# Kernel optimization log

Measured on AMD Instinct MI355X. Metric: run time of the kernel, lower is better.

## Reference

```python
import jax, jax.numpy as jnp
import numpy as np

B, T, D, H, E, O = 4, 2048, 512, 2048, 4, 512
C = 1024  # expert capacity
HE = H // E  # per-expert hidden width


def setup_inputs() -> dict:
    key = jax.random.key(0)
    ks = jax.random.split(key, 7)
    x = jax.random.normal(ks[0], (B, T, D), dtype=jnp.float32)
    dispatch_mask = jax.random.uniform(ks[1], (B, T, E, C), dtype=jnp.float32)
    combine_array = jax.random.uniform(ks[2], (B, T, E, C), dtype=jnp.float32)
    # per-expert parameters (fc1 contract, fc2 expand)
    w1 = jax.random.normal(ks[3], (E, D, HE), dtype=jnp.float32) * (1.0 / np.sqrt(D))
    b1 = jnp.zeros((E, HE), dtype=jnp.float32)
    w2 = jax.random.normal(ks[4], (E, HE, O), dtype=jnp.float32) * (1.0 / np.sqrt(HE))
    b2 = jnp.zeros((O,), dtype=jnp.float32)
    return {"x": x, "dispatch_mask": dispatch_mask, "combine_array": combine_array,
            "w1": w1, "b1": b1, "w2": w2, "b2": b2}


def reference(x, dispatch_mask, combine_array, w1, b1, w2, b2):
    # dispatch: gather tokens into per-expert capacity buffers [B,E,C,D]
    xd = jnp.einsum('btd,btec->becd', x, dispatch_mask)
    # per-expert fc1: [B,E,C,HE]
    h = jnp.einsum('becd,edh->bech', xd, w1) + b1[None, :, None, :]
    # GELU (exact erf form, matching torch nn.GELU default); norm/dropout are identity
    h = jax.nn.gelu(h, approximate=False)
    # per-expert fc2: [B,E,C,O]
    y = jnp.einsum('bech,eho->beco', h, w2)
    # combine: scatter expert outputs back to tokens [B,T,O]
    out = jnp.einsum('beco,btec->bto', y, combine_array) + b2
    return out
```

## Files before the change

### kernel.cpp

```cpp
#include <hip/hip_runtime.h>
#include <math.h>

namespace {

typedef short short8 __attribute__((ext_vector_type(8)));
typedef float f32x4 __attribute__((ext_vector_type(4)));

constexpr int kB = 4, kT = 2048, kD = 512, kE = 4, kC = 1024, kHE = 512,
              kO = 512, kEC = 4096;

__device__ __forceinline__ unsigned short f2bf(float f) {
    unsigned int u = __float_as_uint(f);
    u += 0x7fffu + ((u >> 16) & 1u);
    return (unsigned short)(u >> 16);
}

__device__ __forceinline__ float gelu_exact(float v) {
    return 0.5f * v * (1.0f + erff(v * 0.70710678118654752f));
}

#define GLDS16(g, l)                                                      \
    __builtin_amdgcn_global_load_lds(                                     \
        (const __attribute__((address_space(1))) unsigned int*)(g),       \
        (__attribute__((address_space(3))) unsigned int*)(l), 16, 0, 0)

__global__ __launch_bounds__(256)
void transpose_cast(const float* __restrict__ in, unsigned short* __restrict__ out,
                    int R, int Cc, long long sIn, long long sOut)
{
    __shared__ float tile[32][33];
    const int z = blockIdx.z;
    const float* ip = in + (long long)z * sIn;
    unsigned short* op = out + (long long)z * sOut;
    const int c0 = blockIdx.x * 32, r0 = blockIdx.y * 32;
    const int tx = threadIdx.x & 31, ty = threadIdx.x >> 5;
#pragma unroll
    for (int i = 0; i < 4; ++i) {
        const int r = ty + i * 8;
        tile[r][tx] = ip[(size_t)(r0 + r) * Cc + c0 + tx];
    }
    __syncthreads();
#pragma unroll
    for (int i = 0; i < 4; ++i) {
        const int c = ty + i * 8;
        op[(size_t)(c0 + c) * R + r0 + tx] = f2bf(tile[tx][c]);
    }
}

__global__ __launch_bounds__(256)
void cast_bf16(const float* __restrict__ in, unsigned short* __restrict__ out,
               long long n)
{
    const long long i = ((long long)blockIdx.x * blockDim.x + threadIdx.x) * 4;
    if (i < n) {
        const float4 v = *(const float4*)&in[i];
        unsigned short o[4] = {f2bf(v.x), f2bf(v.y), f2bf(v.z), f2bf(v.w)};
        *(uint2*)&out[i] = *(const uint2*)o;
    }
}

template <int MODE>
__global__ __launch_bounds__(256)
void mfma_gemm(const unsigned short* __restrict__ Aall,
               const unsigned short* __restrict__ Ball,
               const float* __restrict__ biasAll,
               void* __restrict__ Call,
               int M, int N, int K,
               long long sA, long long sB, long long sC,
               int zModA, int zModB, int zModBias, int biasStride, int bShift)
{
    __shared__ unsigned short As[128 * 64];
    __shared__ unsigned short Bs[128 * 64];

    const int z = blockIdx.z;
    const unsigned short* Ab = Aall + (long long)(z % zModA) * sA;
    const unsigned short* Bb = Ball + (long long)(z % zModB) * sB;
    const float* bias =
        (MODE != 0) ? biasAll + (long long)(z % zModBias) * biasStride : nullptr;

    const int t = threadIdx.x;
    const int lane = t & 63;
    const int w = t >> 6;
    const int wrow = w * 32;
    const int l8r = lane >> 3;
    const int l8c = (lane & 7) * 8;
    const int row0 = blockIdx.y * 128;
    const int col0 = blockIdx.x * 128;

    const int wm = (w >> 1) * 64;
    const int wn = (w & 1) * 64;
    const int fr = lane & 15;
    const int fq = (lane >> 4) * 8;

    const unsigned int bMask = (1u << bShift) - 1u;

    f32x4 acc[4][4] = {};

    for (int k0 = 0; k0 < K; k0 += 64) {
#pragma unroll
        for (int r = 0; r < 4; ++r) {
            const int ar = row0 + wrow + r * 8 + l8r;
            GLDS16(Ab + (size_t)ar * K + (k0 + l8c), &As[(wrow + r * 8) * 64]);
            const int bn = col0 + wrow + r * 8 + l8r;
            const int gk = k0 + l8c;
            const size_t boff =
                (((size_t)(gk >> bShift) * N + bn) << bShift) + (gk & bMask);
            GLDS16(Bb + boff, &Bs[(wrow + r * 8) * 64]);
        }
        __syncthreads();
#pragma unroll
        for (int kk = 0; kk < 2; ++kk) {
            short8 af[4], bf[4];
#pragma unroll
            for (int i = 0; i < 4; ++i)
                af[i] = *(const short8*)&As[(wm + i * 16 + fr) * 64 + kk * 32 + fq];
#pragma unroll
            for (int j = 0; j < 4; ++j)
                bf[j] = *(const short8*)&Bs[(wn + j * 16 + fr) * 64 + kk * 32 + fq];
#pragma unroll
            for (int i = 0; i < 4; ++i)
#pragma unroll
                for (int j = 0; j < 4; ++j)
                    acc[i][j] = __builtin_amdgcn_mfma_f32_16x16x32_bf16(
                        af[i], bf[j], acc[i][j], 0, 0, 0);
        }
        __syncthreads();
    }

    const long long cz = (long long)z * sC;
#pragma unroll
    for (int i = 0; i < 4; ++i) {
        const int rowb = row0 + wm + i * 16 + (lane >> 4) * 4;
#pragma unroll
        for (int j = 0; j < 4; ++j) {
            const int col = col0 + wn + j * 16 + fr;
            const float bv = (MODE != 0) ? bias[col] : 0.0f;
#pragma unroll
            for (int r = 0; r < 4; ++r) {
                const float v = acc[i][j][r];
                const size_t idx = (size_t)cz + (size_t)(rowb + r) * N + col;
                if (MODE == 0)
                    ((unsigned short*)Call)[idx] = f2bf(v);
                else if (MODE == 1)
                    ((unsigned short*)Call)[idx] = f2bf(gelu_exact(v + bv));
                else
                    ((float*)Call)[idx] = v + bv;
            }
        }
    }
}

}

extern "C" void kernel_launch(void* const* d_in, const int* in_sizes, int n_in,
                              void* d_out, int out_size, void* d_ws, size_t ws_size,
                              hipStream_t stream)
{
    const float* x    = (const float*)d_in[0];
    const float* mask = (const float*)d_in[1];
    const float* comb = (const float*)d_in[2];
    const float* w1   = (const float*)d_in[3];
    const float* b1   = (const float*)d_in[4];
    const float* w2   = (const float*)d_in[5];
    const float* b2   = (const float*)d_in[6];
    float* out = (float*)d_out;

    unsigned short* ws    = (unsigned short*)d_ws;
    unsigned short* regA  = ws;
    unsigned short* xT    = regA + 33554432;
    unsigned short* w1T   = xT + 4194304;
    unsigned short* w2T   = w1T + 1048576;
    unsigned short* xd    = w2T + 1048576;
    unsigned short* h     = xd + 8388608;
    unsigned short* maskT = regA;
    unsigned short* combB = regA;
    unsigned short* yT    = xd;

    dim3 blk(256);

    transpose_cast<<<dim3(kEC / 32, kT / 32, kB), blk, 0, stream>>>(
        mask, maskT, kT, kEC, (long long)kT * kEC, (long long)kT * kEC);
    transpose_cast<<<dim3(kD / 32, kT / 32, kB), blk, 0, stream>>>(
        x, xT, kT, kD, (long long)kT * kD, (long long)kT * kD);
    transpose_cast<<<dim3(kHE / 32, kD / 32, kE), blk, 0, stream>>>(
        w1, w1T, kD, kHE, (long long)kD * kHE, (long long)kD * kHE);
    transpose_cast<<<dim3(kO / 32, kHE / 32, kE), blk, 0, stream>>>(
        w2, w2T, kHE, kO, (long long)kHE * kO, (long long)kHE * kO);

    mfma_gemm<0><<<dim3(kD / 128, kEC / 128, kB), blk, 0, stream>>>(
        maskT, xT, nullptr, xd, kEC, kD, kT,
        (long long)kEC * kT, (long long)kD * kT, (long long)kEC * kD,
        kB, kB, 1, 0, 11);

    cast_bf16<<<dim3(33554432 / 4 / 256), blk, 0, stream>>>(
        comb, combB, 33554432LL);

    mfma_gemm<1><<<dim3(kHE / 128, kC / 128, kB * kE), blk, 0, stream>>>(
        xd, w1T, b1, h, kC, kHE, kD,
        (long long)kC * kD, (long long)kHE * kD, (long long)kC * kHE,
        kB * kE, kE, kE, kHE, 9);

    mfma_gemm<0><<<dim3(kC / 128, kO / 128, kB * kE), blk, 0, stream>>>(
        w2T, h, nullptr, yT, kO, kC, kHE,
        (long long)kO * kHE, (long long)kC * kHE, (long long)kO * kC,
        kE, kB * kE, 1, 0, 9);

    mfma_gemm<3><<<dim3(kO / 128, kT / 128, kB), blk, 0, stream>>>(
        combB, yT, b2, out, kT, kO, kEC,
        (long long)kT * kEC, (long long)kE * kO * kC, (long long)kT * kO,
        kB, kB, 1, 0, 10);
}
```

Before: 500.3 us.

## Double-buffer GEMM LDS tiles with async prefetch and XOR-swizzled layout

Adds a second LDS buffer for the A and B tiles so the global-to-LDS loads for the next K tile are issued before computing the current one, with explicit vmcnt waits and raw barriers in place of __syncthreads. The LDS layout is also XOR-swizzled on the 16-byte column chunk to reduce bank conflicts on the MFMA fragment reads. Launch bounds request two blocks per CU. LDS use doubles to 64KB per block, which may limit occupancy, and the hand-written waitcnt counts must match the number of issued loads.

```diff
diff --git a/kernel.cpp b/kernel.cpp
--- a/kernel.cpp
+++ b/kernel.cpp
@@ -60,7 +60,7 @@
 }
 
 template <int MODE>
-__global__ __launch_bounds__(256)
+__global__ __launch_bounds__(256, 2)
 void mfma_gemm(const unsigned short* __restrict__ Aall,
                const unsigned short* __restrict__ Ball,
                const float* __restrict__ biasAll,
@@ -69,8 +69,8 @@
                long long sA, long long sB, long long sC,
                int zModA, int zModB, int zModBias, int biasStride, int bShift)
 {
-    __shared__ unsigned short As[128 * 64];
-    __shared__ unsigned short Bs[128 * 64];
+    __shared__ unsigned short As[2][128 * 64];
+    __shared__ unsigned short Bs[2][128 * 64];
 
     const int z = blockIdx.z;
     const unsigned short* Ab = Aall + (long long)(z % zModA) * sA;
@@ -83,7 +83,7 @@
     const int w = t >> 6;
     const int wrow = w * 32;
     const int l8r = lane >> 3;
-    const int l8c = (lane & 7) * 8;
+    const int l8c = ((lane & 7) ^ l8r) * 8;
     const int row0 = blockIdx.y * 128;
     const int col0 = blockIdx.x * 128;
 
@@ -91,32 +91,49 @@
     const int wn = (w & 1) * 64;
     const int fr = lane & 15;
     const int fq = (lane >> 4) * 8;
+    const int fsw = (fr & 7) * 8;
 
     const unsigned int bMask = (1u << bShift) - 1u;
 
     f32x4 acc[4][4] = {};
 
-    for (int k0 = 0; k0 < K; k0 += 64) {
-#pragma unroll
-        for (int r = 0; r < 4; ++r) {
-            const int ar = row0 + wrow + r * 8 + l8r;
-            GLDS16(Ab + (size_t)ar * K + (k0 + l8c), &As[(wrow + r * 8) * 64]);
-            const int bn = col0 + wrow + r * 8 + l8r;
-            const int gk = k0 + l8c;
-            const size_t boff =
-                (((size_t)(gk >> bShift) * N + bn) << bShift) + (gk & bMask);
-            GLDS16(Bb + boff, &Bs[(wrow + r * 8) * 64]);
+#define STAGE(buf, k0)                                                        \
+    do {                                                                      \
+        _Pragma("unroll")                                                     \
+        for (int r = 0; r < 4; ++r) {                                         \
+            const int ar = row0 + wrow + r * 8 + l8r;                         \
+            GLDS16(Ab + (size_t)ar * K + ((k0) + l8c),                        \
+                   &As[buf][(wrow + r * 8) * 64]);                            \
+            const int bn = col0 + wrow + r * 8 + l8r;                         \
+            const int gk = (k0) + l8c;                                        \
+            const size_t boff =                                               \
+                (((size_t)(gk >> bShift) * N + bn) << bShift) + (gk & bMask); \
+            GLDS16(Bb + boff, &Bs[buf][(wrow + r * 8) * 64]);                 \
+        }                                                                     \
+    } while (0)
+
+    const int nt = K / 64;
+    STAGE(0, 0);
+    int cur = 0;
+    for (int t0 = 0; t0 < nt; ++t0) {
+        if (t0 + 1 < nt) {
+            STAGE(cur ^ 1, (t0 + 1) * 64);
+            asm volatile("s_waitcnt vmcnt(8)" ::: "memory");
+        } else {
+            asm volatile("s_waitcnt vmcnt(0)" ::: "memory");
         }
-        __syncthreads();
+        __builtin_amdgcn_s_barrier();
 #pragma unroll
         for (int kk = 0; kk < 2; ++kk) {
             short8 af[4], bf[4];
 #pragma unroll
             for (int i = 0; i < 4; ++i)
-                af[i] = *(const short8*)&As[(wm + i * 16 + fr) * 64 + kk * 32 + fq];
+                af[i] = *(const short8*)&As[cur][(wm + i * 16 + fr) * 64 +
+                                                 ((kk * 32 + fq) ^ fsw)];
 #pragma unroll
             for (int j = 0; j < 4; ++j)
-                bf[j] = *(const short8*)&Bs[(wn + j * 16 + fr) * 64 + kk * 32 + fq];
+                bf[j] = *(const short8*)&Bs[cur][(wn + j * 16 + fr) * 64 +
+                                                 ((kk * 32 + fq) ^ fsw)];
 #pragma unroll
             for (int i = 0; i < 4; ++i)
 #pragma unroll
@@ -124,8 +141,12 @@
                     acc[i][j] = __builtin_amdgcn_mfma_f32_16x16x32_bf16(
                         af[i], bf[j], acc[i][j], 0, 0, 0);
         }
-        __syncthreads();
-    }
+        asm volatile("s_waitcnt lgkmcnt(0)" ::: "memory");
+        __builtin_amdgcn_sched_barrier(0);
+        __builtin_amdgcn_s_barrier();
+        cur ^= 1;
+    }
+#undef STAGE
 
     const long long cz = (long long)z * sC;
 #pragma unroll
```

Measured after the change: 477.2 us. 4.6% less time.
